# Kernel tuning notes

Hardware: AMD Instinct MI355X
Metric: run time of the kernel (lower is better)

The kernel has to match this reference:

```python
import jax, jax.numpy as jnp
import numpy as np

N = 100000      # nodes
E = 1600000     # edges
F_IN = 512      # num_feat
HID = 128       # hidden dim (hardcoded in GNN)
ENC = 64        # encoder_dim
NCLS = 10       # num_classes
DOM = 40        # domain head hidden (hardcoded)


def setup_inputs() -> dict:
    key = jax.random.key(0)
    ks = jax.random.split(key, 16)
    def lin(k, fi, fo):
        kw, kb = jax.random.split(k)
        s = 1.0 / np.sqrt(fi)
        return (jax.random.uniform(kw, (fi, fo), jnp.float32, -s, s),
                jax.random.uniform(kb, (fo,), jnp.float32, -s, s))
    W1, b1 = lin(ks[0], F_IN, HID)
    W2, b2 = lin(ks[1], HID, ENC)
    att_w, att_b = lin(ks[2], ENC, 1)
    cls_w, cls_b = lin(ks[3], ENC, NCLS)
    dw1, db1 = lin(ks[4], ENC, DOM)
    dw2, db2 = lin(ks[5], DOM, 2)
    return {
        "x": jax.random.normal(ks[6], (N, F_IN), jnp.float32),
        "edge_index": jax.random.randint(ks[7], (2, E), 0, N, jnp.int64),
        "ppmi_edge_weight": jax.random.uniform(ks[8], (E,), jnp.float32, 0.01, 1.0),
        "rate": 1,
        "W1": W1, "b1": b1, "W2": W2, "b2": b2,
        "att_w": att_w, "att_b": att_b,
        "cls_w": cls_w, "cls_b": cls_b,
        "dw1": dw1, "db1": db1, "dw2": dw2, "db2": db2,
    }


def _edge_norm(src, dst, w):
    # symmetric normalization d^-1/2 * w * d^-1/2 (self-loops already included)
    deg = jax.ops.segment_sum(w, dst, num_segments=N)
    dinv = jnp.where(deg > 0, jax.lax.rsqrt(deg), 0.0)
    return dinv[src] * w * dinv[dst]


def _conv(h, W, b, src, dst, enorm):
    h = h @ W                                   # [N, out]
    msg = h[src] * enorm[:, None]               # [E+N, out] gather
    return jax.ops.segment_sum(msg, dst, num_segments=N) + b


def _encode(x, src, dst, enorm, W1, b1, W2, b2):
    h = jax.nn.relu(_conv(x, W1, b1, src, dst, enorm))  # dropout = identity (eval)
    return _conv(h, W2, b2, src, dst, enorm)


def reference(x, edge_index, ppmi_edge_weight, rate,
              W1, b1, W2, b2, att_w, att_b,
              cls_w, cls_b, dw1, db1, dw2, db2):
    loop = jnp.arange(N, dtype=edge_index.dtype)
    src = jnp.concatenate([edge_index[0], loop])
    dst = jnp.concatenate([edge_index[1], loop])
    ones_w = jnp.ones(src.shape[0], jnp.float32)
    ppmi_w = jnp.concatenate([ppmi_edge_weight, jnp.ones(N, jnp.float32)])

    gcn_norm = _edge_norm(src, dst, ones_w)
    ppmi_norm = _edge_norm(src, dst, ppmi_w)

    # both encoders share weights (base_model=self.encoder)
    g = _encode(x, src, dst, gcn_norm, W1, b1, W2, b2)    # [N, ENC]
    p = _encode(x, src, dst, ppmi_norm, W1, b1, W2, b2)   # [N, ENC]

    stacked = jnp.stack([g, p], axis=1)                   # [N, 2, ENC]
    logits = stacked @ att_w + att_b                      # [N, 2, 1]
    wts = jax.nn.softmax(logits, axis=1)
    emb = jnp.sum(stacked * wts, axis=1)                  # [N, ENC]

    class_predict = emb @ cls_w + cls_b
    r = jnp.float32(rate)
    # gradient reversal: identity fwd, -rate * grad bwd
    rev = jax.lax.stop_gradient((1.0 + r) * emb) - r * emb
    h = jax.nn.relu(rev @ dw1 + db1)                      # dropout = identity (eval)
    domain_predict = h @ dw2 + db2
    return emb, class_predict, domain_predict
```

## Files before the change

### kernel.cpp

```cpp
#include <hip/hip_runtime.h>
#include <math.h>
#include <stdint.h>

#define NND  100000
#define NED  1600000
#define FIN  512
#define HID  128
#define ENC  64
#define NCLS 10
#define DOM  40

#define SCAN_BS 256
#define NBS ((NND + SCAN_BS - 1) / SCAN_BS)

#define NDEG   96
#define NGEMM  782
#define NPH1   (NGEMM + NDEG)

typedef __attribute__((ext_vector_type(8))) short short8v;
typedef __attribute__((ext_vector_type(8))) unsigned short ushort8v;
typedef __attribute__((ext_vector_type(4))) float f32x4;
typedef __attribute__((ext_vector_type(4))) unsigned int uint4v;


__device__ inline void split8(const float4 a, const float4 b,
                              short8v& hi, short8v& lo) {
  float f[8] = {a.x, a.y, a.z, a.w, b.x, b.y, b.z, b.w};
  uint4v H, L;
#pragma unroll
  for (int i = 0; i < 4; ++i) {
    unsigned int u0 = __float_as_uint(f[2 * i]);
    unsigned int u1 = __float_as_uint(f[2 * i + 1]);
    H[i] = (u0 >> 16) | (u1 & 0xffff0000u);
    float l0 = f[2 * i]     - __uint_as_float(u0 & 0xffff0000u);
    float l1 = f[2 * i + 1] - __uint_as_float(u1 & 0xffff0000u);
    L[i] = (__float_as_uint(l0) >> 16) | (__float_as_uint(l1) & 0xffff0000u);
  }
  hi = __builtin_bit_cast(short8v, H);
  lo = __builtin_bit_cast(short8v, L);
}

__device__ inline ushort f2bf_rne(float x) {
  unsigned int u = __float_as_uint(x);
  unsigned int r = u + 0x7fffu + ((u >> 16) & 1u);
  return (ushort)(r >> 16);
}

__device__ inline float bf2f(unsigned short v) {
  return __uint_as_float((unsigned int)v << 16);
}

__device__ inline void gload_lds16(const float* gp, float* lp) {
  __builtin_amdgcn_global_load_lds(
      (const __attribute__((address_space(1))) void*)gp,
      (__attribute__((address_space(3))) void*)lp, 16, 0, 0);
}


__global__ void k_bprep2(const float* __restrict__ W1, ushort* __restrict__ b1hi,
                         ushort* __restrict__ b1lo, const float* __restrict__ W2,
                         ushort* __restrict__ b2hi, ushort* __restrict__ b2lo) {
  int id = blockIdx.x * 256 + threadIdx.x;
  const float* B; ushort *bhi, *blo; int NC;
  if (id < FIN * HID) { B = W1; bhi = b1hi; blo = b1lo; NC = HID; }
  else {
    id -= FIN * HID;
    if (id >= HID * ENC) return;
    B = W2; bhi = b2hi; blo = b2lo; NC = ENC;
  }
  int k = id / NC, c = id % NC;
  float x = B[id];
  unsigned int u = __float_as_uint(x);
  ushort h = (ushort)(u >> 16);
  float lo = x - __uint_as_float(u & 0xffff0000u);
  ushort l = (ushort)(__float_as_uint(lo) >> 16);
  size_t o = ((size_t)(k >> 3) * NC + c) * 8 + (k & 7);
  bhi[o] = h;
  blo[o] = l;
}


__global__ __launch_bounds__(256, 3) void k_phase1(
    const float* __restrict__ A, const ushort* __restrict__ Bhi,
    const ushort* __restrict__ Blo, ushort* __restrict__ C,
    const int* __restrict__ dst, const float* __restrict__ ppmi,
    unsigned long long* __restrict__ packed, int* __restrict__ rank) {
  __shared__ float At[2][128 * 32];
  const int bi = blockIdx.x;

  if ((bi & 7) == 7 && bi < 768) {
    int dbi = bi >> 3;
    for (int e = dbi * 256 + threadIdx.x; e < NED; e += NDEG * 256) {
      int d = dst[e];
      unsigned int fx = (unsigned int)(ppmi[e] * 1073741824.0f + 0.5f);
      unsigned long long v = (1ull << 40) | (unsigned long long)fx;
      unsigned long long old = atomicAdd(&packed[d], v);
      rank[e] = (int)(old >> 40);
    }
    return;
  }

  const int gb = (bi < 768) ? (bi - (bi >> 3)) : (bi - NDEG);
  const int tid = threadIdx.x;
  const int lane = tid & 63;
  const int w = tid >> 6;
  const int wr = w >> 1, wc = w & 1;
  const int g = lane >> 4;
  const int l16 = lane & 15;
  const int row_base = gb * 128;

  size_t srow[4]; int scol[4];
  {
    int e = w * 256 + lane * 4;
#pragma unroll
    for (int i = 0; i < 4; ++i) {
      int ee = e + i * 1024;
      int r = ee >> 5;
      int chunk_lds = (ee >> 2) & 7;
      int chunk_g = chunk_lds ^ (r & 7);
      int rr = row_base + r; if (rr >= NND) rr = NND - 1;
      srow[i] = (size_t)rr * FIN;
      scol[i] = chunk_g * 4;
    }
  }

  int coln[4];
#pragma unroll
  for (int n = 0; n < 4; ++n) coln[n] = wc * 64 + n * 16 + l16;
  int arow_l[4];
#pragma unroll
  for (int m = 0; m < 4; ++m) arow_l[m] = wr * 64 + m * 16 + l16;

  f32x4 acc[4][4] = {};

#pragma unroll
  for (int i = 0; i < 4; ++i)
    gload_lds16(A + srow[i] + 0 + scol[i], &At[0][w * 256 + i * 1024]);
  __syncthreads();

  for (int t = 0; t < FIN / 32; ++t) {
    const int cur = t & 1;
    if (t + 1 < FIN / 32) {
      const int k0n = (t + 1) * 32;
#pragma unroll
      for (int i = 0; i < 4; ++i)
        gload_lds16(A + srow[i] + k0n + scol[i], &At[cur ^ 1][w * 256 + i * 1024]);
    }

    short8v ah[4], al[4];
#pragma unroll
    for (int m = 0; m < 4; ++m) {
      int r = arow_l[m];
      int c0 = (((g * 2)     ^ (r & 7)) << 2);
      int c1 = (((g * 2 + 1) ^ (r & 7)) << 2);
      float4 a0 = *(const float4*)&At[cur][r * 32 + c0];
      float4 a1 = *(const float4*)&At[cur][r * 32 + c1];
      split8(a0, a1, ah[m], al[m]);
    }

    short8v bh[4], bl[4];
    const int kc = t * 4 + g;
#pragma unroll
    for (int n = 0; n < 4; ++n) {
      size_t off = ((size_t)kc * HID + coln[n]) * 8;
      bh[n] = *(const short8v*)(Bhi + off);
      bl[n] = *(const short8v*)(Blo + off);
    }

#pragma unroll
    for (int m = 0; m < 4; ++m)
#pragma unroll
      for (int n = 0; n < 4; ++n) {
        acc[m][n] = __builtin_amdgcn_mfma_f32_16x16x32_bf16(ah[m], bh[n], acc[m][n], 0, 0, 0);
        acc[m][n] = __builtin_amdgcn_mfma_f32_16x16x32_bf16(al[m], bh[n], acc[m][n], 0, 0, 0);
        acc[m][n] = __builtin_amdgcn_mfma_f32_16x16x32_bf16(ah[m], bl[n], acc[m][n], 0, 0, 0);
      }

    __syncthreads();
  }

#pragma unroll
  for (int m = 0; m < 4; ++m)
#pragma unroll
    for (int i = 0; i < 4; ++i) {
      int r = row_base + wr * 64 + m * 16 + g * 4 + i;
      if (r < NND) {
#pragma unroll
        for (int n = 0; n < 4; ++n)
          C[(size_t)r * HID + coln[n]] = f2bf_rne(acc[m][n][i]);
      }
    }
}


__global__ void k_dinv_scan(const unsigned long long* __restrict__ packed,
                            float* __restrict__ dinv_g, float* __restrict__ dinv_p,
                            int* __restrict__ psum) {
  __shared__ int s[SCAN_BS];
  int t = threadIdx.x, i = blockIdx.x * SCAN_BS + t;
  int cnt = 0;
  if (i < NND) {
    unsigned long long pk = packed[i];
    cnt = (int)(pk >> 40);
    float dp = (float)(pk & 0xFFFFFFFFFFull) * (1.0f / 1073741824.0f);
    dinv_g[i] = 1.0f / sqrtf((float)cnt + 1.0f);
    dinv_p[i] = 1.0f / sqrtf(dp + 1.0f);
  }
  s[t] = cnt;
  __syncthreads();
  for (int o = SCAN_BS / 2; o; o >>= 1) {
    if (t < o) s[t] += s[t + o];
    __syncthreads();
  }
  if (t == 0) psum[blockIdx.x] = s[0];
}

__global__ void k_scan_b(int* __restrict__ psum) {
  __shared__ int s[512];
  int t = threadIdx.x;
  int v = (t < NBS) ? psum[t] : 0;
  s[t] = v;
  __syncthreads();
  for (int o = 1; o < 512; o <<= 1) {
    int add = (t >= o) ? s[t - o] : 0;
    __syncthreads();
    s[t] += add;
    __syncthreads();
  }
  if (t < NBS) psum[t] = s[t] - v;
}

__global__ void k_scan_c(const unsigned long long* __restrict__ packed,
                         const int* __restrict__ psum, int* __restrict__ row_ptr) {
  __shared__ int s[SCAN_BS];
  int t = threadIdx.x, i = blockIdx.x * SCAN_BS + t;
  int v = (i < NND) ? (int)(packed[i] >> 40) : 0;
  s[t] = v;
  __syncthreads();
  for (int o = 1; o < SCAN_BS; o <<= 1) {
    int add = (t >= o) ? s[t - o] : 0;
    __syncthreads();
    s[t] += add;
    __syncthreads();
  }
  if (i < NND) row_ptr[i] = psum[blockIdx.x] + s[t] - v;
  if (i == NND - 1) row_ptr[NND] = psum[blockIdx.x] + s[t];
}


__global__ void k_scatter(const int* __restrict__ src, const int* __restrict__ dst,
                          const float* __restrict__ ppmi,
                          const int* __restrict__ row_ptr, const int* __restrict__ rank,
                          const float* __restrict__ dinv_g, const float* __restrict__ dinv_p,
                          int2* __restrict__ csr) {
  int e = blockIdx.x * blockDim.x + threadIdx.x;
  if (e >= NED) return;
  int s = src[e], d = dst[e];
  int pos = row_ptr[d] + rank[e];
  ushort gn = f2bf_rne(dinv_g[s] * dinv_g[d]);
  ushort pn = f2bf_rne(dinv_p[s] * ppmi[e] * dinv_p[d]);
  int2 rec;
  rec.x = s;
  rec.y = (int)gn | ((int)pn << 16);
  csr[pos] = rec;
}


template<int WR>
__global__ __launch_bounds__(256, 4) void gemm2_split(
    const ushort* __restrict__ As, const ushort* __restrict__ Bhi,
    const ushort* __restrict__ Blo, ushort* __restrict__ C,
    int M, int K, int Nc) {
  const int lane = threadIdx.x & 63;
  const int w = threadIdx.x >> 6;
  const int g = lane >> 4;
  const int l16 = lane & 15;
  const int row_base = blockIdx.x * (WR * 64) + w * 64;

  size_t arow[4];
#pragma unroll
  for (int m = 0; m < 4; ++m) {
    int r = row_base + m * 16 + l16;
    if (r >= M) r = M - 1;
    arow[m] = (size_t)r * K;
  }
  int coln[4];
#pragma unroll
  for (int n = 0; n < 4; ++n) coln[n] = n * 16 + l16;

  f32x4 acc[4][4] = {};

  for (int k0 = 0; k0 < K; k0 += 32) {
    short8v ah[4];
#pragma unroll
    for (int m = 0; m < 4; ++m)
      ah[m] = *(const short8v*)(As + arow[m] + k0 + g * 8);
    short8v bh[4], bl[4];
    const int kc = (k0 >> 3) + g;
#pragma unroll
    for (int n = 0; n < 4; ++n) {
      size_t off = ((size_t)kc * Nc + coln[n]) * 8;
      bh[n] = *(const short8v*)(Bhi + off);
      bl[n] = *(const short8v*)(Blo + off);
    }
#pragma unroll
    for (int m = 0; m < 4; ++m)
#pragma unroll
      for (int n = 0; n < 4; ++n) {
        acc[m][n] = __builtin_amdgcn_mfma_f32_16x16x32_bf16(ah[m], bh[n], acc[m][n], 0, 0, 0);
        acc[m][n] = __builtin_amdgcn_mfma_f32_16x16x32_bf16(ah[m], bl[n], acc[m][n], 0, 0, 0);
      }
  }

#pragma unroll
  for (int m = 0; m < 4; ++m)
#pragma unroll
    for (int i = 0; i < 4; ++i) {
      int r = row_base + m * 16 + g * 4 + i;
      if (r < M) {
#pragma unroll
        for (int n = 0; n < 4; ++n) {
          int c = coln[n];
          size_t o = (r < NND) ? ((size_t)r * 128 + c)
                               : ((size_t)(r - NND) * 128 + 64 + c);
          C[o] = f2bf_rne(acc[m][n][i]);
        }
      }
    }
}


__global__ __launch_bounds__(256) void k_agg1(
    const ushort* __restrict__ hlinb, const int* __restrict__ row_ptr,
    const int2* __restrict__ csr,
    const float* __restrict__ dinv_g, const float* __restrict__ dinv_p,
    const float* __restrict__ b1, ushort* __restrict__ hhs) {
  int wid = (blockIdx.x * blockDim.x + threadIdx.x) >> 6;
  int lane = threadIdx.x & 63;
  if (wid >= NND) return;
  const int gp = lane >> 4;
  const int t  = lane & 15;
  float sg = dinv_g[wid]; sg *= sg;
  float sp = dinv_p[wid]; sp *= sp;

  float ag[8] = {}, ap[8] = {};
  if (gp == 0) {
    ushort8v v = *(const ushort8v*)(hlinb + (size_t)wid * HID + 8 * t);
#pragma unroll
    for (int i = 0; i < 8; ++i) {
      float f = bf2f(v[i]);
      ag[i] = f * sg; ap[i] = f * sp;
    }
  }
  int e0 = row_ptr[wid], e1 = row_ptr[wid + 1];
  int k = e0 + gp;
  if (k < e1) {
    int2 rec = csr[k];
    while (true) {
      int kn = k + 4;
      int2 nrec = csr[kn < e1 ? kn : k];
      float wg = bf2f((ushort)(rec.y & 0xffff));
      float wp = bf2f((ushort)((unsigned)rec.y >> 16));
      ushort8v u = *(const ushort8v*)(hlinb + (size_t)rec.x * HID + 8 * t);
#pragma unroll
      for (int i = 0; i < 8; ++i) {
        float f = bf2f(u[i]);
        ag[i] = fmaf(f, wg, ag[i]);
        ap[i] = fmaf(f, wp, ap[i]);
      }
      if (kn >= e1) break;
      k = kn; rec = nrec;
    }
  }
#pragma unroll
  for (int i = 0; i < 8; ++i) {
    ag[i] += __shfl_xor(ag[i], 32); ap[i] += __shfl_xor(ap[i], 32);
    ag[i] += __shfl_xor(ag[i], 16); ap[i] += __shfl_xor(ap[i], 16);
  }

  float bb[8];
  *(float4*)&bb[0] = *(const float4*)(b1 + 8 * t);
  *(float4*)&bb[4] = *(const float4*)(b1 + 8 * t + 4);
  if (gp == 0 || gp == 2) {
    ushort8v outv;
#pragma unroll
    for (int i = 0; i < 8; ++i) {
      float v = (gp == 0) ? fmaxf(ag[i] + bb[i], 0.f) : fmaxf(ap[i] + bb[i], 0.f);
      outv[i] = f2bf_rne(v);
    }
    size_t row = (gp == 0) ? (size_t)wid : (size_t)(NND + wid);
    *(ushort8v*)(hhs + row * HID + 8 * t) = outv;
  }
}


__global__ __launch_bounds__(256) void k_agg2(
    const ushort* __restrict__ h2b, const int* __restrict__ row_ptr,
    const int2* __restrict__ csr,
    const float* __restrict__ dinv_g, const float* __restrict__ dinv_p,
    const float* __restrict__ b2, const float* __restrict__ att_w,
    const float* __restrict__ att_b, float* __restrict__ out_emb) {
  int wid = (blockIdx.x * blockDim.x + threadIdx.x) >> 6;
  int lane = threadIdx.x & 63;
  if (wid >= NND) return;
  const int gp = lane >> 4;
  const int t  = lane & 15;
  const int br = t >> 3;
  const int f0 = (t & 7) * 8;
  float sg = dinv_g[wid]; sg *= sg;
  float sp = dinv_p[wid]; sp *= sp;
  const float sw = br ? sp : sg;

  float acc[8] = {};
  if (gp == 0) {
    ushort8v v = *(const ushort8v*)(h2b + (size_t)wid * 128 + 8 * t);
#pragma unroll
    for (int i = 0; i < 8; ++i) acc[i] = bf2f(v[i]) * sw;
  }
  int e0 = row_ptr[wid], e1 = row_ptr[wid + 1];
  int k = e0 + gp;
  if (k < e1) {
    int2 rec = csr[k];
    while (true) {
      int kn = k + 4;
      int2 nrec = csr[kn < e1 ? kn : k];
      float w = br ? bf2f((ushort)((unsigned)rec.y >> 16))
                   : bf2f((ushort)(rec.y & 0xffff));
      ushort8v u = *(const ushort8v*)(h2b + (size_t)rec.x * 128 + 8 * t);
#pragma unroll
      for (int i = 0; i < 8; ++i) acc[i] = fmaf(bf2f(u[i]), w, acc[i]);
      if (kn >= e1) break;
      k = kn; rec = nrec;
    }
  }
#pragma unroll
  for (int i = 0; i < 8; ++i) {
    acc[i] += __shfl_xor(acc[i], 32);
    acc[i] += __shfl_xor(acc[i], 16);
  }

  float bb[8];
  *(float4*)&bb[0] = *(const float4*)(b2 + f0);
  *(float4*)&bb[4] = *(const float4*)(b2 + f0 + 4);
  float v[8];
#pragma unroll
  for (int i = 0; i < 8; ++i) v[i] = acc[i] + bb[i];

  float aw[8];
  *(float4*)&aw[0] = *(const float4*)(att_w + f0);
  *(float4*)&aw[4] = *(const float4*)(att_w + f0 + 4);
  float part = 0.f;
#pragma unroll
  for (int i = 0; i < 8; ++i) part = fmaf(v[i], aw[i], part);
  part += __shfl_xor(part, 4);
  part += __shfl_xor(part, 2);
  part += __shfl_xor(part, 1);
  float other = __shfl_xor(part, 8);
  float ab = att_b[0];
  float lg = (br ? other : part) + ab;
  float lp = (br ? part : other) + ab;
  float mx = fmaxf(lg, lp);
  float eg = expf(lg - mx), ep2 = expf(lp - mx);
  float wsm = eg / (eg + ep2);

  float ov[8];
#pragma unroll
  for (int i = 0; i < 8; ++i) ov[i] = __shfl_xor(v[i], 8);
  if (gp == 0 && br == 0) {
    float4* dst = (float4*)(out_emb + (size_t)wid * 64 + f0);
    float4 o0, o1;
    o0.x = wsm * v[0] + (1.f - wsm) * ov[0];
    o0.y = wsm * v[1] + (1.f - wsm) * ov[1];
    o0.z = wsm * v[2] + (1.f - wsm) * ov[2];
    o0.w = wsm * v[3] + (1.f - wsm) * ov[3];
    o1.x = wsm * v[4] + (1.f - wsm) * ov[4];
    o1.y = wsm * v[5] + (1.f - wsm) * ov[5];
    o1.z = wsm * v[6] + (1.f - wsm) * ov[6];
    o1.w = wsm * v[7] + (1.f - wsm) * ov[7];
    dst[0] = o0;
    dst[1] = o1;
  }
}


__global__ __launch_bounds__(128) void k_head(
    const float* __restrict__ emb,
    const float* __restrict__ cls_w, const float* __restrict__ cls_b,
    const float* __restrict__ dw1, const float* __restrict__ db1,
    const float* __restrict__ dw2, const float* __restrict__ db2,
    float* __restrict__ out_cls, float* __restrict__ out_dom) {
  __shared__ float se[128 * 65];
  const int t = threadIdx.x;
  const int base = blockIdx.x * 128;
  for (int c = 0; c < 64; ++c) {
    int idx = c * 128 + t;
    int nl = idx >> 6, k = idx & 63;
    size_t g = (size_t)base * ENC + idx;
    float v = (g < (size_t)NND * ENC) ? emb[g] : 0.f;
    se[nl * 65 + k] = v;
  }
  __syncthreads();

  int node = base + t;
  float c[NCLS], hd[DOM];
#pragma unroll
  for (int j = 0; j < NCLS; ++j) c[j] = cls_b[j];
#pragma unroll
  for (int j = 0; j < DOM; ++j) hd[j] = db1[j];

  for (int k = 0; k < ENC; ++k) {
    float ev = se[t * 65 + k];
#pragma unroll
    for (int j = 0; j < NCLS; ++j) c[j] += ev * cls_w[k * NCLS + j];
#pragma unroll
    for (int j = 0; j < DOM; ++j) hd[j] += ev * dw1[k * DOM + j];
  }
  float d0 = db2[0], d1 = db2[1];
#pragma unroll
  for (int j = 0; j < DOM; ++j) {
    float hv = fmaxf(hd[j], 0.f);
    d0 += hv * dw2[j * 2];
    d1 += hv * dw2[j * 2 + 1];
  }
  if (node < NND) {
#pragma unroll
    for (int j = 0; j < NCLS; ++j) out_cls[(size_t)node * NCLS + j] = c[j];
    out_dom[(size_t)node * 2]     = d0;
    out_dom[(size_t)node * 2 + 1] = d1;
  }
}


extern "C" void kernel_launch(void* const* d_in, const int* in_sizes, int n_in,
                              void* d_out, int out_size, void* d_ws, size_t ws_size,
                              hipStream_t stream) {
  const float* x     = (const float*)d_in[0];
  const int*   ei    = (const int*)d_in[1];
  const float* ppmi  = (const float*)d_in[2];
  const float* W1    = (const float*)d_in[4];
  const float* b1    = (const float*)d_in[5];
  const float* W2    = (const float*)d_in[6];
  const float* b2    = (const float*)d_in[7];
  const float* att_w = (const float*)d_in[8];
  const float* att_b = (const float*)d_in[9];
  const float* cls_w = (const float*)d_in[10];
  const float* cls_b = (const float*)d_in[11];
  const float* dw1   = (const float*)d_in[12];
  const float* db1   = (const float*)d_in[13];
  const float* dw2   = (const float*)d_in[14];
  const float* db2   = (const float*)d_in[15];

  const int* src = ei;
  const int* dst = ei + NED;

  uintptr_t p = (uintptr_t)d_ws;
  auto alloc = [&](size_t bytes) -> void* {
    void* r = (void*)p;
    p += (bytes + 255) & ~(size_t)255;
    return r;
  };
  unsigned long long* packed = (unsigned long long*)alloc((size_t)NND * 8);
  int*    rank    = (int*)   alloc((size_t)NED * 4);
  int*    row_ptr = (int*)   alloc((size_t)(NND + 1) * 4);
  int*    psum    = (int*)   alloc((size_t)NBS * 4);
  float*  dinv_g  = (float*) alloc((size_t)NND * 4);
  float*  dinv_p  = (float*) alloc((size_t)NND * 4);
  int2*   csr     = (int2*)  alloc((size_t)NED * 8);
  ushort* b1hi    = (ushort*)alloc((size_t)FIN * HID * 2);
  ushort* b1lo    = (ushort*)alloc((size_t)FIN * HID * 2);
  ushort* b2hi    = (ushort*)alloc((size_t)HID * ENC * 2);
  ushort* b2lo    = (ushort*)alloc((size_t)HID * ENC * 2);
  ushort* h2b     = (ushort*)alloc((size_t)NND * HID * 2);
  ushort* hhs     = (ushort*)alloc((size_t)2 * NND * HID * 2);

  float* out_emb = (float*)d_out;
  float* out_cls = (float*)d_out + (size_t)NND * ENC;
  float* out_dom = (float*)d_out + (size_t)NND * (ENC + NCLS);

  ushort* h_linb = (ushort*)d_out;

  hipMemsetAsync(packed, 0, (size_t)NND * 8, stream);
  k_bprep2<<<(FIN * HID + HID * ENC + 255) / 256, 256, 0, stream>>>(
      W1, b1hi, b1lo, W2, b2hi, b2lo);

  k_phase1<<<NPH1, 256, 0, stream>>>(x, b1hi, b1lo, h_linb,
                                     dst, ppmi, packed, rank);

  k_dinv_scan<<<NBS, SCAN_BS, 0, stream>>>(packed, dinv_g, dinv_p, psum);
  k_scan_b<<<1, 512, 0, stream>>>(psum);
  k_scan_c<<<NBS, SCAN_BS, 0, stream>>>(packed, psum, row_ptr);
  k_scatter<<<NED / 256, 256, 0, stream>>>(src, dst, ppmi, row_ptr, rank,
                                           dinv_g, dinv_p, csr);

  k_agg1<<<(NND * 64) / 256, 256, 0, stream>>>(h_linb, row_ptr, csr,
                                               dinv_g, dinv_p, b1, hhs);
  gemm2_split<4><<<(2 * NND + 255) / 256, 256, 0, stream>>>(
      hhs, b2hi, b2lo, h2b, 2 * NND, HID, ENC);
  k_agg2<<<(NND * 64) / 256, 256, 0, stream>>>(h2b, row_ptr, csr,
                                               dinv_g, dinv_p, b2, att_w, att_b, out_emb);

  k_head<<<(NND + 127) / 128, 128, 0, stream>>>(out_emb, cls_w, cls_b, dw1, db1,
                                                dw2, db2, out_cls, out_dom);
}
```

Baseline: 465.1 us.

## Split fused degree/GEMM phase into separate kernels and fold memset into prep

Replaces the combined kernel that interleaved atomic degree/rank blocks with GEMM1 blocks by a standalone atomic degree kernel and a separate GEMM1 kernel with higher occupancy bounds. It also zeroes the packed degree array inside the weight-prep kernel instead of a separate memset, and raises gemm2 launch bounds. This removes a launch and lets each kernel tune occupancy independently, at the cost of losing concurrent overlap between the atomic pass and the GEMM.

```diff
diff --git a/kernel.cpp b/kernel.cpp
--- a/kernel.cpp
+++ b/kernel.cpp
@@ -13,10 +13,6 @@
 #define SCAN_BS 256
 #define NBS ((NND + SCAN_BS - 1) / SCAN_BS)
 
-#define NDEG   96
-#define NGEMM  782
-#define NPH1   (NGEMM + NDEG)
-
 typedef __attribute__((ext_vector_type(8))) short short8v;
 typedef __attribute__((ext_vector_type(8))) unsigned short ushort8v;
 typedef __attribute__((ext_vector_type(4))) float f32x4;
@@ -57,10 +53,12 @@
 }
 
 
-__global__ void k_bprep2(const float* __restrict__ W1, ushort* __restrict__ b1hi,
-                         ushort* __restrict__ b1lo, const float* __restrict__ W2,
-                         ushort* __restrict__ b2hi, ushort* __restrict__ b2lo) {
+__global__ void k_prep(const float* __restrict__ W1, ushort* __restrict__ b1hi,
+                       ushort* __restrict__ b1lo, const float* __restrict__ W2,
+                       ushort* __restrict__ b2hi, ushort* __restrict__ b2lo,
+                       unsigned long long* __restrict__ packed) {
   int id = blockIdx.x * 256 + threadIdx.x;
+  if (id < NND) packed[id] = 0ull;
   const float* B; ushort *bhi, *blo; int NC;
   if (id < FIN * HID) { B = W1; bhi = b1hi; blo = b1lo; NC = HID; }
   else {
@@ -80,116 +78,16 @@
 }
 
 
-__global__ __launch_bounds__(256, 3) void k_phase1(
-    const float* __restrict__ A, const ushort* __restrict__ Bhi,
-    const ushort* __restrict__ Blo, ushort* __restrict__ C,
-    const int* __restrict__ dst, const float* __restrict__ ppmi,
-    unsigned long long* __restrict__ packed, int* __restrict__ rank) {
-  __shared__ float At[2][128 * 32];
-  const int bi = blockIdx.x;
-
-  if ((bi & 7) == 7 && bi < 768) {
-    int dbi = bi >> 3;
-    for (int e = dbi * 256 + threadIdx.x; e < NED; e += NDEG * 256) {
-      int d = dst[e];
-      unsigned int fx = (unsigned int)(ppmi[e] * 1073741824.0f + 0.5f);
-      unsigned long long v = (1ull << 40) | (unsigned long long)fx;
-      unsigned long long old = atomicAdd(&packed[d], v);
-      rank[e] = (int)(old >> 40);
-    }
-    return;
-  }
-
-  const int gb = (bi < 768) ? (bi - (bi >> 3)) : (bi - NDEG);
-  const int tid = threadIdx.x;
-  const int lane = tid & 63;
-  const int w = tid >> 6;
-  const int wr = w >> 1, wc = w & 1;
-  const int g = lane >> 4;
-  const int l16 = lane & 15;
-  const int row_base = gb * 128;
-
-  size_t srow[4]; int scol[4];
-  {
-    int e = w * 256 + lane * 4;
-#pragma unroll
-    for (int i = 0; i < 4; ++i) {
-      int ee = e + i * 1024;
-      int r = ee >> 5;
-      int chunk_lds = (ee >> 2) & 7;
-      int chunk_g = chunk_lds ^ (r & 7);
-      int rr = row_base + r; if (rr >= NND) rr = NND - 1;
-      srow[i] = (size_t)rr * FIN;
-      scol[i] = chunk_g * 4;
-    }
-  }
-
-  int coln[4];
-#pragma unroll
-  for (int n = 0; n < 4; ++n) coln[n] = wc * 64 + n * 16 + l16;
-  int arow_l[4];
-#pragma unroll
-  for (int m = 0; m < 4; ++m) arow_l[m] = wr * 64 + m * 16 + l16;
-
-  f32x4 acc[4][4] = {};
-
-#pragma unroll
-  for (int i = 0; i < 4; ++i)
-    gload_lds16(A + srow[i] + 0 + scol[i], &At[0][w * 256 + i * 1024]);
-  __syncthreads();
-
-  for (int t = 0; t < FIN / 32; ++t) {
-    const int cur = t & 1;
-    if (t + 1 < FIN / 32) {
-      const int k0n = (t + 1) * 32;
-#pragma unroll
-      for (int i = 0; i < 4; ++i)
-        gload_lds16(A + srow[i] + k0n + scol[i], &At[cur ^ 1][w * 256 + i * 1024]);
-    }
-
-    short8v ah[4], al[4];
-#pragma unroll
-    for (int m = 0; m < 4; ++m) {
-      int r = arow_l[m];
-      int c0 = (((g * 2)     ^ (r & 7)) << 2);
-      int c1 = (((g * 2 + 1) ^ (r & 7)) << 2);
-      float4 a0 = *(const float4*)&At[cur][r * 32 + c0];
-      float4 a1 = *(const float4*)&At[cur][r * 32 + c1];
-      split8(a0, a1, ah[m], al[m]);
-    }
-
-    short8v bh[4], bl[4];
-    const int kc = t * 4 + g;
-#pragma unroll
-    for (int n = 0; n < 4; ++n) {
-      size_t off = ((size_t)kc * HID + coln[n]) * 8;
-      bh[n] = *(const short8v*)(Bhi + off);
-      bl[n] = *(const short8v*)(Blo + off);
-    }
-
-#pragma unroll
-    for (int m = 0; m < 4; ++m)
-#pragma unroll
-      for (int n = 0; n < 4; ++n) {
-        acc[m][n] = __builtin_amdgcn_mfma_f32_16x16x32_bf16(ah[m], bh[n], acc[m][n], 0, 0, 0);
-        acc[m][n] = __builtin_amdgcn_mfma_f32_16x16x32_bf16(al[m], bh[n], acc[m][n], 0, 0, 0);
-        acc[m][n] = __builtin_amdgcn_mfma_f32_16x16x32_bf16(ah[m], bl[n], acc[m][n], 0, 0, 0);
-      }
-
-    __syncthreads();
-  }
-
-#pragma unroll
-  for (int m = 0; m < 4; ++m)
-#pragma unroll
-    for (int i = 0; i < 4; ++i) {
-      int r = row_base + wr * 64 + m * 16 + g * 4 + i;
-      if (r < NND) {
-#pragma unroll
-        for (int n = 0; n < 4; ++n)
-          C[(size_t)r * HID + coln[n]] = f2bf_rne(acc[m][n][i]);
-      }
-    }
+__global__ void k_deg_rank(const int* __restrict__ dst, const float* __restrict__ ppmi,
+                           unsigned long long* __restrict__ packed,
+                           int* __restrict__ rank) {
+  int e = blockIdx.x * blockDim.x + threadIdx.x;
+  if (e >= NED) return;
+  int d = dst[e];
+  unsigned int fx = (unsigned int)(ppmi[e] * 1073741824.0f + 0.5f);
+  unsigned long long v = (1ull << 40) | (unsigned long long)fx;
+  unsigned long long old = atomicAdd(&packed[d], v);
+  rank[e] = (int)(old >> 40);
 }
 
 
@@ -266,8 +164,104 @@
 }
 
 
+__global__ __launch_bounds__(256, 4) void gemm1_lds(
+    const float* __restrict__ A, const ushort* __restrict__ Bhi,
+    const ushort* __restrict__ Blo, ushort* __restrict__ C) {
+  __shared__ float At[2][128 * 32];
+  const int tid = threadIdx.x;
+  const int lane = tid & 63;
+  const int w = tid >> 6;
+  const int wr = w >> 1, wc = w & 1;
+  const int g = lane >> 4;
+  const int l16 = lane & 15;
+  const int row_base = blockIdx.x * 128;
+
+  size_t srow[4]; int scol[4];
+  {
+    int e = w * 256 + lane * 4;
+#pragma unroll
+    for (int i = 0; i < 4; ++i) {
+      int ee = e + i * 1024;
+      int r = ee >> 5;
+      int chunk_lds = (ee >> 2) & 7;
+      int chunk_g = chunk_lds ^ (r & 7);
+      int rr = row_base + r; if (rr >= NND) rr = NND - 1;
+      srow[i] = (size_t)rr * FIN;
+      scol[i] = chunk_g * 4;
+    }
+  }
+
+  int coln[4];
+#pragma unroll
+  for (int n = 0; n < 4; ++n) coln[n] = wc * 64 + n * 16 + l16;
+  int arow_l[4];
+#pragma unroll
+  for (int m = 0; m < 4; ++m) arow_l[m] = wr * 64 + m * 16 + l16;
+
+  f32x4 acc[4][4] = {};
+
+#pragma unroll
+  for (int i = 0; i < 4; ++i)
+    gload_lds16(A + srow[i] + 0 + scol[i], &At[0][w * 256 + i * 1024]);
+  __syncthreads();
+
+  for (int t = 0; t < FIN / 32; ++t) {
+    const int cur = t & 1;
+    if (t + 1 < FIN / 32) {
+      const int k0n = (t + 1) * 32;
+#pragma unroll
+      for (int i = 0; i < 4; ++i)
+        gload_lds16(A + srow[i] + k0n + scol[i], &At[cur ^ 1][w * 256 + i * 1024]);
+    }
+
+    short8v ah[4], al[4];
+#pragma unroll
+    for (int m = 0; m < 4; ++m) {
+      int r = arow_l[m];
+      int c0 = (((g * 2)     ^ (r & 7)) << 2);
+      int c1 = (((g * 2 + 1) ^ (r & 7)) << 2);
+      float4 a0 = *(const float4*)&At[cur][r * 32 + c0];
+      float4 a1 = *(const float4*)&At[cur][r * 32 + c1];
+      split8(a0, a1, ah[m], al[m]);
+    }
+
+    short8v bh[4], bl[4];
+    const int kc = t * 4 + g;
+#pragma unroll
+    for (int n = 0; n < 4; ++n) {
+      size_t off = ((size_t)kc * HID + coln[n]) * 8;
+      bh[n] = *(const short8v*)(Bhi + off);
+      bl[n] = *(const short8v*)(Blo + off);
+    }
+
+#pragma unroll
+    for (int m = 0; m < 4; ++m)
+#pragma unroll
+      for (int n = 0; n < 4; ++n) {
+        acc[m][n] = __builtin_amdgcn_mfma_f32_16x16x32_bf16(ah[m], bh[n], acc[m][n], 0, 0, 0);
+        acc[m][n] = __builtin_amdgcn_mfma_f32_16x16x32_bf16(al[m], bh[n], acc[m][n], 0, 0, 0);
+        acc[m][n] = __builtin_amdgcn_mfma_f32_16x16x32_bf16(ah[m], bl[n], acc[m][n], 0, 0, 0);
+      }
+
+    __syncthreads();
+  }
+
+#pragma unroll
+  for (int m = 0; m < 4; ++m)
+#pragma unroll
+    for (int i = 0; i < 4; ++i) {
+      int r = row_base + wr * 64 + m * 16 + g * 4 + i;
+      if (r < NND) {
+#pragma unroll
+        for (int n = 0; n < 4; ++n)
+          C[(size_t)r * HID + coln[n]] = f2bf_rne(acc[m][n][i]);
+      }
+    }
+}
+
+
 template<int WR>
-__global__ __launch_bounds__(256, 4) void gemm2_split(
+__global__ __launch_bounds__(256, 6) void gemm2_split(
     const ushort* __restrict__ As, const ushort* __restrict__ Bhi,
     const ushort* __restrict__ Blo, ushort* __restrict__ C,
     int M, int K, int Nc) {
@@ -579,19 +573,17 @@
 
   ushort* h_linb = (ushort*)d_out;
 
-  hipMemsetAsync(packed, 0, (size_t)NND * 8, stream);
-  k_bprep2<<<(FIN * HID + HID * ENC + 255) / 256, 256, 0, stream>>>(
-      W1, b1hi, b1lo, W2, b2hi, b2lo);
-
-  k_phase1<<<NPH1, 256, 0, stream>>>(x, b1hi, b1lo, h_linb,
-                                     dst, ppmi, packed, rank);
-
+  k_prep<<<(NND + 255) / 256, 256, 0, stream>>>(W1, b1hi, b1lo, W2, b2hi, b2lo,
+                                                packed);
+
+  k_deg_rank<<<NED / 256, 256, 0, stream>>>(dst, ppmi, packed, rank);
   k_dinv_scan<<<NBS, SCAN_BS, 0, stream>>>(packed, dinv_g, dinv_p, psum);
   k_scan_b<<<1, 512, 0, stream>>>(psum);
   k_scan_c<<<NBS, SCAN_BS, 0, stream>>>(packed, psum, row_ptr);
   k_scatter<<<NED / 256, 256, 0, stream>>>(src, dst, ppmi, row_ptr, rank,
                                            dinv_g, dinv_p, csr);
 
+  gemm1_lds<<<(NND + 127) / 128, 256, 0, stream>>>(x, b1hi, b1lo, h_linb);
   k_agg1<<<(NND * 64) / 256, 256, 0, stream>>>(h_linb, row_ptr, csr,
                                                dinv_g, dinv_p, b1, hhs);
   gemm2_split<4><<<(2 * NND + 255) / 256, 256, 0, stream>>>(
```

After: 547.6 us. 17.8% more time.
